# Kernel tuning notes

Measured on AMD Instinct MI355X. Metric: run time of the kernel, lower is better.

Reference implementation:

```python
import jax, jax.numpy as jnp
import numpy as np

D_STATE = 8
HIDDEN = 256


def _neighbor_sum(x):
    # frozen depthwise 3x3 conv, all-ones kernel with zero center, padding=1
    B, C, H, W = x.shape
    xp = jnp.pad(x, ((0, 0), (0, 0), (1, 1), (1, 1)))
    full = sum(xp[:, :, di:di + H, dj:dj + W] for di in range(3) for dj in range(3))
    return full - x  # subtract center tap


def setup_inputs() -> dict:
    key = jax.random.key(0)
    ks = jax.random.split(key, 6)
    B, H, W = 4, 256, 256
    c_in = 2 * D_STATE          # 16
    c_nbr = c_in * 8            # 128
    c_out = 8 * D_STATE         # 64
    s = 0.05
    return {
        "x_cat": jax.random.normal(ks[0], (B, c_in, H, W), dtype=jnp.float32),
        "w1": jax.random.normal(ks[1], (HIDDEN, c_nbr), dtype=jnp.float32) * s,
        "w2": jax.random.normal(ks[2], (HIDDEN, HIDDEN), dtype=jnp.float32) * s,
        "w3": jax.random.normal(ks[3], (HIDDEN, HIDDEN), dtype=jnp.float32) * s,
        "w4": jax.random.normal(ks[4], (HIDDEN, HIDDEN), dtype=jnp.float32) * s,
        "w5": jax.random.normal(ks[5], (c_out, HIDDEN), dtype=jnp.float32) * s,
    }


def reference(x_cat, w1, w2, w3, w4, w5):
    B, C, H, W = x_cat.shape
    d_state = C // 2
    # depthwise stencil: each of the 8 out-channels per group is the same neighbor sum
    nbr = _neighbor_sum(x_cat)                      # [B, 2d, H, W]
    xn = jnp.repeat(nbr, 8, axis=1)                 # [B, 16d, H, W]
    # five 1x1 convs with interleaved ELU (per-pixel MLP)
    h = jax.nn.elu(jnp.einsum('bchw,oc->bohw', xn, w1))
    h = jax.nn.elu(jnp.einsum('bchw,oc->bohw', h, w2))
    h = jax.nn.elu(jnp.einsum('bchw,oc->bohw', h, w3))
    h = jax.nn.elu(jnp.einsum('bchw,oc->bohw', h, w4))
    F_int = jnp.einsum('bchw,oc->bohw', h, w5)      # [B, 8d, H, W]
    d4 = 4 * d_state
    real = F_int[:, :d4].reshape(B, 4, d_state, H, W).mean(axis=1) * 0.1
    imag = F_int[:, d4:].reshape(B, 4, d_state, H, W).mean(axis=1) * 0.1
    return jnp.concatenate([real, imag], axis=1)    # [B, 2d, H, W]
```

## Files before the change

kernel.cpp:

```cpp
#include <hip/hip_runtime.h>

typedef __attribute__((ext_vector_type(8))) short bf16x8;
typedef __attribute__((ext_vector_type(4))) float f32x4;

__device__ __forceinline__ unsigned int f2bf(float f) {
  unsigned int u = __builtin_bit_cast(unsigned int, f);
  return (u + 0x7FFFu + ((u >> 16) & 1u)) >> 16;
}
__device__ __forceinline__ float eluf(float x) {
  return x > 0.f ? x : (__expf(x) - 1.f);
}
__device__ __forceinline__ unsigned int cvt_pk_bf16(float a, float b) {
  unsigned int r;
  asm("v_cvt_pk_bf16_f32 %0, %1, %2" : "=v"(r) : "v"(a), "v"(b));
  return r;
}

__global__ __launch_bounds__(256) void prep_kernel(
    const float* __restrict__ w1, const float* __restrict__ w2,
    const float* __restrict__ w3, const float* __restrict__ w4,
    const float* __restrict__ w5, unsigned short* __restrict__ ws) {
  int idx = blockIdx.x * 256 + threadIdx.x;
  float v = 0.f;
  if (idx < 8192) {
    int mt = idx >> 9, l = (idx >> 3) & 63, j = idx & 7;
    int o = mt * 16 + (l & 15), c = (l >> 4) * 8 + j;
    if (c < 16) {
      const float* r = w1 + o * 128 + c * 8;
      v = ((r[0] + r[1]) + (r[2] + r[3])) + ((r[4] + r[5]) + (r[6] + r[7]));
    }
  } else if (idx < 204800) {
    int t = idx - 8192;
    int which = t >> 16, e = t & 65535;
    const float* w = (which == 0) ? w2 : (which == 1) ? w3 : w4;
    int mt = e >> 12, kt = (e >> 9) & 7, l = (e >> 3) & 63, j = e & 7;
    int o = mt * 16 + (l & 15), c = kt * 32 + (l >> 4) * 8 + j;
    v = w[o * 256 + c];
  } else {
    int e = idx - 204800;
    int kt = e >> 9, l = (e >> 3) & 63, j = e & 7;
    int d = l & 15, c = kt * 32 + (l >> 4) * 8 + j;
    float s = 0.f;
    if (d < 8) {
      for (int g = 0; g < 4; ++g) s += w5[(g * 8 + d) * 256 + c];
    } else {
      for (int g = 0; g < 4; ++g) s += w5[(32 + g * 8 + (d - 8)) * 256 + c];
    }
    v = 0.025f * s;
  }
  ws[idx] = (unsigned short)f2bf(v);
}

#define ACT0 33792

__global__ __launch_bounds__(512, 4) void qca_kernel(
    const float* __restrict__ xcat, const unsigned short* __restrict__ wsu,
    float* __restrict__ out) {
  __shared__ __align__(16) char lds[38912];
  float* xt = reinterpret_cast<float*>(lds);

  const int tid = threadIdx.x;
  const int w = tid >> 6, l = tid & 63;
  const int l15 = l & 15, lhi = l >> 4;
  const int wm = w >> 1, wn = w & 1;

  const int tile = blockIdx.x << 6;
  const int bimg = tile >> 16;
  const int y = (tile >> 8) & 255;
  const int x0 = tile & 255;

  for (int t = tid; t < 16 * 3 * 66; t += 512) {
    int c = t / 198;
    int rem = t - c * 198;
    int rr = rem / 66;
    int xl = rem - rr * 66;
    int gy = y + rr - 1, gx = x0 + xl - 1;
    float v = 0.f;
    if (gy >= 0 && gy < 256 && gx >= 0 && gx < 256)
      v = xcat[(size_t)(bimg * 16 + c) * 65536 + gy * 256 + gx];
    xt[t] = v;
  }
  __syncthreads();

  for (int t = tid; t < 2048; t += 512) {
    int p = t & 63, c = t >> 6;
    float v = 0.f;
    if (c < 16) {
      const float* bp = xt + c * 198 + (p + 1);
      v = (bp[-1] + bp[0] + bp[1]) + (bp[65] + bp[67]) +
          (bp[131] + bp[132] + bp[133]);
    }
    reinterpret_cast<unsigned short*>(lds + ACT0)[p * 40 + c] =
        (unsigned short)f2bf(v);
  }
  __syncthreads();

  const int px = wn * 32 + l15;
  const int lb_r = px * 528 + lhi * 16;
  const int lb_w = px * 528 + wm * 128 + lhi * 8;
  const int lb_a1 = px * 80 + lhi * 16;

  f32x4 acc[4][2];

  auto epi = [&]() {
#pragma unroll
    for (int mi = 0; mi < 4; ++mi)
#pragma unroll
      for (int ni = 0; ni < 2; ++ni) {
        f32x4 v = acc[mi][ni];
        unsigned int u01 = cvt_pk_bf16(eluf(v[0]), eluf(v[1]));
        unsigned int u23 = cvt_pk_bf16(eluf(v[2]), eluf(v[3]));
        *reinterpret_cast<uint2*>(lds + lb_w + (ni * 8448 + mi * 32)) =
            uint2{u01, u23};
      }
  };

  {
#pragma unroll
    for (int mi = 0; mi < 4; ++mi)
#pragma unroll
      for (int ni = 0; ni < 2; ++ni) acc[mi][ni] = f32x4{0.f, 0.f, 0.f, 0.f};
    const bf16x8* w1v = reinterpret_cast<const bf16x8*>(wsu);
    bf16x8 bq[2];
#pragma unroll
    for (int ni = 0; ni < 2; ++ni)
      bq[ni] = *reinterpret_cast<const bf16x8*>(lds + ACT0 + lb_a1 + ni * 1280);
#pragma unroll
    for (int mi = 0; mi < 4; ++mi) {
      bf16x8 a = w1v[((wm << 2) + mi) * 64 + l];
#pragma unroll
      for (int ni = 0; ni < 2; ++ni)
        acc[mi][ni] = __builtin_amdgcn_mfma_f32_16x16x32_bf16(
            a, bq[ni], acc[mi][ni], 0, 0, 0);
    }
    epi();
    __syncthreads();
  }

  auto mid = [&](const unsigned short* wbase) {
    const bf16x8* wv = reinterpret_cast<const bf16x8*>(wbase);
#pragma unroll
    for (int mi = 0; mi < 4; ++mi)
#pragma unroll
      for (int ni = 0; ni < 2; ++ni) acc[mi][ni] = f32x4{0.f, 0.f, 0.f, 0.f};
#pragma unroll
    for (int kt = 0; kt < 8; ++kt) {
      bf16x8 bq[2];
#pragma unroll
      for (int ni = 0; ni < 2; ++ni)
        bq[ni] = *reinterpret_cast<const bf16x8*>(
            lds + lb_r + (ni * 8448 + kt * 64));
#pragma unroll
      for (int mi = 0; mi < 4; ++mi) {
        bf16x8 a = wv[(((wm << 2) + mi) * 8 + kt) * 64 + l];
#pragma unroll
        for (int ni = 0; ni < 2; ++ni)
          acc[mi][ni] = __builtin_amdgcn_mfma_f32_16x16x32_bf16(
              a, bq[ni], acc[mi][ni], 0, 0, 0);
      }
    }
    __syncthreads();
    epi();
    __syncthreads();
  };

  mid(wsu + 8192);
  mid(wsu + 73728);
  mid(wsu + 139264);

  if (w < 4) {
    const bf16x8* w5v = reinterpret_cast<const bf16x8*>(wsu + 204800);
    f32x4 a5 = f32x4{0.f, 0.f, 0.f, 0.f};
    const int p = (w << 4) + l15;
    const int lb5 = p * 528 + lhi * 16;
#pragma unroll
    for (int kt = 0; kt < 8; ++kt) {
      bf16x8 a = w5v[kt * 64 + l];
      bf16x8 b = *reinterpret_cast<const bf16x8*>(lds + lb5 + kt * 64);
      a5 = __builtin_amdgcn_mfma_f32_16x16x32_bf16(a, b, a5, 0, 0, 0);
    }
    int pix = tile + p;
    int rem = pix & 65535;
    float* op = out + (size_t)(pix >> 16) * 1048576 + rem;
#pragma unroll
    for (int r = 0; r < 4; ++r) op[(lhi * 4 + r) * 65536] = a5[r];
  }
}

extern "C" void kernel_launch(void* const* d_in, const int* in_sizes, int n_in,
                              void* d_out, int out_size, void* d_ws,
                              size_t ws_size, hipStream_t stream) {
  const float* xcat = (const float*)d_in[0];
  const float* w1 = (const float*)d_in[1];
  const float* w2 = (const float*)d_in[2];
  const float* w3 = (const float*)d_in[3];
  const float* w4 = (const float*)d_in[4];
  const float* w5 = (const float*)d_in[5];
  unsigned short* ws = (unsigned short*)d_ws;
  float* out = (float*)d_out;

  prep_kernel<<<816, 256, 0, stream>>>(w1, w2, w3, w4, w5, ws);
  qca_kernel<<<4096, 512, 0, stream>>>(xcat, ws, out);
}
```

Before: 156.8 us.

## Halve tile to 32 pixels and ping-pong activation buffers to drop a barrier

The per-block tile shrinks from 64 to 32 pixels, with 256 threads in 4 waves where each wave owns a 64-channel output slice, and the grid doubles. Activations now alternate between two LDS buffers across layers, so the barrier before each epilogue write can be removed. In exchange, every block reloads the same weights for half as many pixels, which doubles global and L2 weight traffic per pixel and raises the stencil halo overhead.

```diff
diff --git a/kernel.cpp b/kernel.cpp
--- a/kernel.cpp
+++ b/kernel.cpp
@@ -51,29 +51,29 @@
   ws[idx] = (unsigned short)f2bf(v);
 }
 
-#define ACT0 33792
-
-__global__ __launch_bounds__(512, 4) void qca_kernel(
+#define BUF0 0
+#define BUF1 16896
+
+__global__ __launch_bounds__(256, 4) void qca_kernel(
     const float* __restrict__ xcat, const unsigned short* __restrict__ wsu,
     float* __restrict__ out) {
-  __shared__ __align__(16) char lds[38912];
-  float* xt = reinterpret_cast<float*>(lds);
+  __shared__ __align__(16) char lds[33792];
+  float* xt = reinterpret_cast<float*>(lds + BUF0);
 
   const int tid = threadIdx.x;
   const int w = tid >> 6, l = tid & 63;
   const int l15 = l & 15, lhi = l >> 4;
-  const int wm = w >> 1, wn = w & 1;
-
-  const int tile = blockIdx.x << 6;
+
+  const int tile = blockIdx.x << 5;
   const int bimg = tile >> 16;
   const int y = (tile >> 8) & 255;
   const int x0 = tile & 255;
 
-  for (int t = tid; t < 16 * 3 * 66; t += 512) {
-    int c = t / 198;
-    int rem = t - c * 198;
-    int rr = rem / 66;
-    int xl = rem - rr * 66;
+  for (int t = tid; t < 16 * 3 * 34; t += 256) {
+    int c = t / 102;
+    int rem = t - c * 102;
+    int rr = rem / 34;
+    int xl = rem - rr * 34;
     int gy = y + rr - 1, gx = x0 + xl - 1;
     float v = 0.f;
     if (gy >= 0 && gy < 256 && gx >= 0 && gx < 256)
@@ -82,27 +82,26 @@
   }
   __syncthreads();
 
-  for (int t = tid; t < 2048; t += 512) {
-    int p = t & 63, c = t >> 6;
+  for (int t = tid; t < 1024; t += 256) {
+    int p = t & 31, c = t >> 5;
     float v = 0.f;
     if (c < 16) {
-      const float* bp = xt + c * 198 + (p + 1);
-      v = (bp[-1] + bp[0] + bp[1]) + (bp[65] + bp[67]) +
-          (bp[131] + bp[132] + bp[133]);
-    }
-    reinterpret_cast<unsigned short*>(lds + ACT0)[p * 40 + c] =
+      const float* bp = xt + c * 102 + (p + 1);
+      v = (bp[-1] + bp[0] + bp[1]) + (bp[33] + bp[35]) +
+          (bp[67] + bp[68] + bp[69]);
+    }
+    reinterpret_cast<unsigned short*>(lds + BUF1)[p * 40 + c] =
         (unsigned short)f2bf(v);
   }
   __syncthreads();
 
-  const int px = wn * 32 + l15;
-  const int lb_r = px * 528 + lhi * 16;
-  const int lb_w = px * 528 + wm * 128 + lhi * 8;
-  const int lb_a1 = px * 80 + lhi * 16;
+  const int lb_r = l15 * 528 + lhi * 16;
+  const int lb_w = l15 * 528 + w * 128 + lhi * 8;
+  const int lb_a1 = l15 * 80 + lhi * 16;
 
   f32x4 acc[4][2];
 
-  auto epi = [&]() {
+  auto epi = [&](int dstoff) {
 #pragma unroll
     for (int mi = 0; mi < 4; ++mi)
 #pragma unroll
@@ -110,7 +109,7 @@
         f32x4 v = acc[mi][ni];
         unsigned int u01 = cvt_pk_bf16(eluf(v[0]), eluf(v[1]));
         unsigned int u23 = cvt_pk_bf16(eluf(v[2]), eluf(v[3]));
-        *reinterpret_cast<uint2*>(lds + lb_w + (ni * 8448 + mi * 32)) =
+        *reinterpret_cast<uint2*>(lds + lb_w + (dstoff + ni * 8448 + mi * 32)) =
             uint2{u01, u23};
       }
   };
@@ -124,20 +123,20 @@
     bf16x8 bq[2];
 #pragma unroll
     for (int ni = 0; ni < 2; ++ni)
-      bq[ni] = *reinterpret_cast<const bf16x8*>(lds + ACT0 + lb_a1 + ni * 1280);
+      bq[ni] = *reinterpret_cast<const bf16x8*>(lds + BUF1 + lb_a1 + ni * 1280);
 #pragma unroll
     for (int mi = 0; mi < 4; ++mi) {
-      bf16x8 a = w1v[((wm << 2) + mi) * 64 + l];
+      bf16x8 a = w1v[((w << 2) + mi) * 64 + l];
 #pragma unroll
       for (int ni = 0; ni < 2; ++ni)
         acc[mi][ni] = __builtin_amdgcn_mfma_f32_16x16x32_bf16(
             a, bq[ni], acc[mi][ni], 0, 0, 0);
     }
-    epi();
+    epi(BUF0);
     __syncthreads();
   }
 
-  auto mid = [&](const unsigned short* wbase) {
+  auto mid = [&](int srcoff, int dstoff, const unsigned short* wbase) {
     const bf16x8* wv = reinterpret_cast<const bf16x8*>(wbase);
 #pragma unroll
     for (int mi = 0; mi < 4; ++mi)
@@ -149,26 +148,25 @@
 #pragma unroll
       for (int ni = 0; ni < 2; ++ni)
         bq[ni] = *reinterpret_cast<const bf16x8*>(
-            lds + lb_r + (ni * 8448 + kt * 64));
+            lds + lb_r + (srcoff + ni * 8448 + kt * 64));
 #pragma unroll
       for (int mi = 0; mi < 4; ++mi) {
-        bf16x8 a = wv[(((wm << 2) + mi) * 8 + kt) * 64 + l];
+        bf16x8 a = wv[(((w << 2) + mi) * 8 + kt) * 64 + l];
 #pragma unroll
         for (int ni = 0; ni < 2; ++ni)
           acc[mi][ni] = __builtin_amdgcn_mfma_f32_16x16x32_bf16(
               a, bq[ni], acc[mi][ni], 0, 0, 0);
       }
     }
-    __syncthreads();
-    epi();
+    epi(dstoff);
     __syncthreads();
   };
 
-  mid(wsu + 8192);
-  mid(wsu + 73728);
-  mid(wsu + 139264);
-
-  if (w < 4) {
+  mid(BUF0, BUF1, wsu + 8192);
+  mid(BUF1, BUF0, wsu + 73728);
+  mid(BUF0, BUF1, wsu + 139264);
+
+  if (w < 2) {
     const bf16x8* w5v = reinterpret_cast<const bf16x8*>(wsu + 204800);
     f32x4 a5 = f32x4{0.f, 0.f, 0.f, 0.f};
     const int p = (w << 4) + l15;
@@ -176,7 +174,7 @@
 #pragma unroll
     for (int kt = 0; kt < 8; ++kt) {
       bf16x8 a = w5v[kt * 64 + l];
-      bf16x8 b = *reinterpret_cast<const bf16x8*>(lds + lb5 + kt * 64);
+      bf16x8 b = *reinterpret_cast<const bf16x8*>(lds + BUF1 + lb5 + kt * 64);
       a5 = __builtin_amdgcn_mfma_f32_16x16x32_bf16(a, b, a5, 0, 0, 0);
     }
     int pix = tile + p;
@@ -200,5 +198,5 @@
   float* out = (float*)d_out;
 
   prep_kernel<<<816, 256, 0, stream>>>(w1, w2, w3, w4, w5, ws);
-  qca_kernel<<<4096, 512, 0, stream>>>(xcat, ws, out);
-}
+  qca_kernel<<<8192, 256, 0, stream>>>(xcat, ws, out);
+}
```

Measured after the change: 162.7 us. +3.8%, slower.
